# Kernel optimization log

Measured on AMD Instinct MI355X. Metric: run time of the kernel, lower is better.

The kernel has to match this reference:

```python
import jax, jax.numpy as jnp
import numpy as np


def setup_inputs() -> dict:
    key = jax.random.key(0)
    ks = jax.random.split(key, 7)
    B, Nc, Nt = 4, 2048, 2048
    D = 512          # key_size == representation_size
    H, E = 8, 64     # num_heads, head_dim = D // H
    return {
        "keys": jax.random.normal(ks[0], (B, Nc, D), dtype=jnp.float32),
        "values": jax.random.normal(ks[1], (B, Nc, D), dtype=jnp.float32),
        "query": jax.random.normal(ks[2], (B, Nt, D), dtype=jnp.float32),
        "Wk": jax.random.normal(ks[3], (H, D, E), dtype=jnp.float32) * 0.02,
        "Wv": jax.random.normal(ks[4], (H, D, E), dtype=jnp.float32) * 0.02,
        "Wq": jax.random.normal(ks[5], (H, D, E), dtype=jnp.float32) * 0.02,
        "Wout": jax.random.normal(ks[6], (D, D), dtype=jnp.float32) * 0.02,
    }


def reference(keys, values, query, Wk, Wv, Wq, Wout):
    # Batched per-head projections (replaces the per-head Python loop)
    k = jnp.einsum("bnd,hde->bhne", keys, Wk)    # [B,H,Nc,E]
    v = jnp.einsum("bnd,hde->bhne", values, Wv)  # [B,H,Nc,E]
    q = jnp.einsum("bnd,hde->bhne", query, Wq)   # [B,H,Nt,E]
    head_dim = q.shape[-1]
    # NOTE: original scales by head_dim (query.size()[2]), not sqrt(head_dim)
    scores = jnp.einsum("bhqe,bhke->bhqk", q, k) / head_dim
    attn = jax.nn.softmax(scores, axis=-1)
    out = jnp.einsum("bhqk,bhke->bhqe", attn, v)  # [B,H,Nt,E]
    # concat over heads (head-major feature order, matches torch.cat(dim=-1))
    B, H, Nt, E = out.shape
    out = jnp.transpose(out, (0, 2, 1, 3)).reshape(B, Nt, H * E)
    # final Linear (no bias): x @ Wout^T
    return out @ Wout.T
```

## Files before the change

kernel.cpp:

```cpp
#include <hip/hip_runtime.h>

#define B_   4
#define H_   8
#define NSEQ 2048
#define D_   512
#define E_   64

typedef __bf16 bf16x8 __attribute__((ext_vector_type(8)));
typedef float  f32x4  __attribute__((ext_vector_type(4)));
typedef float  f32x16 __attribute__((ext_vector_type(16)));

__device__ __forceinline__ unsigned short f2b(float f) {
    __bf16 h = (__bf16)f;
    return __builtin_bit_cast(unsigned short, h);
}
__device__ __forceinline__ unsigned pk2(float a, float b) {
    return (unsigned)f2b(a) | ((unsigned)f2b(b) << 16);
}
__device__ __forceinline__ bf16x8 ld_frag(const unsigned short* p) {
    return *reinterpret_cast<const bf16x8*>(p);
}
__device__ __forceinline__ void async_copy16(const void* g, const unsigned short* l) {
    __builtin_amdgcn_global_load_lds(
        (const __attribute__((address_space(1))) unsigned int*)g,
        (__attribute__((address_space(3))) unsigned int*)l, 16, 0, 0);
}

__device__ __forceinline__ int lds_blk(int r, int s) {
    int lr = r >> 1;
    return lr * 128 + (((((r & 1) << 3) | s) ^ (lr & 15)) << 3);
}
#define STAGE_SRC(r0, l, row, slot)                                            \
    {   int lr_ = ((r0) >> 1) + ((l) >> 4);                                    \
        int B_x = ((l) & 15) ^ (lr_ & 15);                                     \
        row = (lr_ << 1) | (B_x >> 3);  slot = B_x & 7; }

__global__ __launch_bounds__(256)
void cast_w_kernel(const float* __restrict__ Wk, const float* __restrict__ Wv,
                   const float* __restrict__ Wq, const float* __restrict__ Wo,
                   unsigned short* __restrict__ okt, unsigned short* __restrict__ ovt,
                   unsigned short* __restrict__ oqt, unsigned short* __restrict__ oo) {
    int idx = blockIdx.x * 256 + threadIdx.x;
    int y = blockIdx.y;
    if (y == 3) { oo[idx] = f2b(Wo[idx]); return; }
    const float* src = y == 0 ? Wk : (y == 1 ? Wv : Wq);
    unsigned short* dst = y == 0 ? okt : (y == 1 ? ovt : oqt);
    float scl = (y == 2) ? 0.015625f : 1.0f;
    int hh = idx >> 15, rem = idx & 32767, d = rem >> 6, e = rem & 63;
    dst[hh * 32768 + e * 512 + d] = f2b(src[idx] * scl);
}

__global__ __launch_bounds__(256)
void xcast_kernel(const float* __restrict__ q, const float* __restrict__ k,
                  const float* __restrict__ v,
                  unsigned short* __restrict__ qx, unsigned short* __restrict__ kx,
                  unsigned short* __restrict__ vx) {
    const int y = blockIdx.y;
    const float* src = y == 0 ? q : (y == 1 ? k : v);
    unsigned short* dst = y == 0 ? qx : (y == 1 ? kx : vx);
    #pragma unroll
    for (int i = 0; i < 4; ++i) {
        int e = blockIdx.x * 4096 + i * 1024 + threadIdx.x * 4;
        float4 f = *reinterpret_cast<const float4*>(src + e);
        *reinterpret_cast<ushort4*>(dst + e) =
            make_ushort4(f2b(f.x), f2b(f.y), f2b(f.z), f2b(f.w));
    }
}

__global__ __launch_bounds__(256, 2)
void proj_gemm(const unsigned short* __restrict__ qx,
               const unsigned short* __restrict__ kx,
               const unsigned short* __restrict__ vx,
               const unsigned short* __restrict__ wqt,
               const unsigned short* __restrict__ wkt,
               const unsigned short* __restrict__ wvt,
               unsigned short* __restrict__ qb, unsigned short* __restrict__ kb,
               unsigned short* __restrict__ vtb) {
    const int m0  = blockIdx.x * 128;
    const int no0 = blockIdx.y * 128;
    const int which = blockIdx.z;
    const int tid = threadIdx.x;
    const int wave = tid >> 6, lane = tid & 63;
    const int quad = lane >> 4, l16 = lane & 15;
    const int wr = wave >> 1, wc = wave & 1;

    const unsigned short* X = which == 0 ? qx : (which == 1 ? kx : vx);
    const unsigned short* W = which == 0 ? wqt : (which == 1 ? wkt : wvt);

    __shared__ unsigned short SM[32768];
    unsigned short* Ab = SM;
    unsigned short* Bb = SM + 16384;

    const unsigned short* Xp = X + (size_t)m0 * D_;
    const unsigned short* Wp = W + (size_t)no0 * D_;

    int rowS[4], slS[4];
    #pragma unroll
    for (int i = 0; i < 4; ++i) STAGE_SRC(wave * 32 + i * 8, lane, rowS[i], slS[i])

    #define PROJ_STAGE(kt, buf)                                                \
        {   _Pragma("unroll")                                                  \
            for (int i = 0; i < 4; ++i)                                        \
                async_copy16(Xp + (size_t)rowS[i] * D_ + (kt) * 64 + slS[i] * 8, \
                             Ab + (buf) * 8192 + (wave * 32 + i * 8) * 64);    \
            _Pragma("unroll")                                                  \
            for (int i = 0; i < 4; ++i)                                        \
                async_copy16(Wp + (size_t)rowS[i] * D_ + (kt) * 64 + slS[i] * 8, \
                             Bb + (buf) * 8192 + (wave * 32 + i * 8) * 64);    \
        }

    PROJ_STAGE(0, 0)
    __syncthreads();

    const f32x4 z = {0.f, 0.f, 0.f, 0.f};
    f32x4 acc[4][4];
    #pragma unroll
    for (int i = 0; i < 4; ++i)
        #pragma unroll
        for (int j = 0; j < 4; ++j) acc[i][j] = z;

    for (int kt = 0; kt < 8; ++kt) {
        const int cur = kt & 1;
        if (kt + 1 < 8) PROJ_STAGE(kt + 1, 1 - cur)
        #pragma unroll
        for (int kk = 0; kk < 2; ++kk) {
            const int s = kk * 4 + quad;
            bf16x8 bfr[4];
            #pragma unroll
            for (int nt = 0; nt < 4; ++nt)
                bfr[nt] = ld_frag(&Bb[cur * 8192 +
                                      lds_blk(wc * 64 + nt * 16 + l16, s)]);
            #pragma unroll
            for (int mt = 0; mt < 4; ++mt) {
                bf16x8 af = ld_frag(&Ab[cur * 8192 +
                                        lds_blk(wr * 64 + mt * 16 + l16, s)]);
                #pragma unroll
                for (int nt = 0; nt < 4; ++nt)
                    acc[mt][nt] = __builtin_amdgcn_mfma_f32_16x16x32_bf16(
                        af, bfr[nt], acc[mt][nt], 0, 0, 0);
            }
        }
        __syncthreads();
    }

    if (which != 2) {
        unsigned short (*Os)[136] = reinterpret_cast<unsigned short(*)[136]>(SM);
        #pragma unroll
        for (int mt = 0; mt < 4; ++mt)
            #pragma unroll
            for (int nt = 0; nt < 4; ++nt)
                #pragma unroll
                for (int r = 0; r < 4; ++r)
                    Os[wr * 64 + mt * 16 + quad * 4 + r][wc * 64 + nt * 16 + l16] =
                        f2b(acc[mt][nt][r]);
        __syncthreads();
        unsigned short* Y = (which == 0 ? qb : kb);
        #pragma unroll
        for (int i = 0; i < 8; ++i) {
            int idx = tid + i * 256;
            int row = idx >> 4, seg = idx & 15;
            *reinterpret_cast<uint4*>(Y + (size_t)(m0 + row) * D_ + no0 + seg * 8) =
                *reinterpret_cast<const uint4*>(&Os[row][seg * 8]);
        }
    } else {
        unsigned short (*Ot)[138] = reinterpret_cast<unsigned short(*)[138]>(SM);
        #pragma unroll
        for (int mt = 0; mt < 4; ++mt)
            #pragma unroll
            for (int nt = 0; nt < 4; ++nt) {
                ushort4 o = make_ushort4(f2b(acc[mt][nt][0]), f2b(acc[mt][nt][1]),
                                         f2b(acc[mt][nt][2]), f2b(acc[mt][nt][3]));
                *reinterpret_cast<ushort4*>(
                    &Ot[wc * 64 + nt * 16 + l16][wr * 64 + mt * 16 + quad * 4]) = o;
            }
        __syncthreads();
        const int b = m0 >> 11, nloc = m0 & 2047;
        #pragma unroll
        for (int i = 0; i < 8; ++i) {
            int idx = tid + i * 256;
            int lhe = idx >> 4, seg = idx & 15;
            int ghe = no0 + lhe;
            *reinterpret_cast<uint4*>(
                vtb + ((size_t)(b * H_ + (ghe >> 6)) * E_ + (ghe & 63)) * NSEQ +
                nloc + seg * 8) =
                *reinterpret_cast<const uint4*>(&Ot[lhe][seg * 8]);
        }
    }
    #undef PROJ_STAGE
}

__global__ __launch_bounds__(256, 3)
void attn_kernel(const unsigned short* __restrict__ qbp,
                 const unsigned short* __restrict__ kbp,
                 const unsigned short* __restrict__ vtbp,
                 unsigned short* __restrict__ aob) {
    const int L = blockIdx.x;
    const int bh = L & 31, qt = L >> 5;
    const int b = bh >> 3, h = bh & 7;
    const int n0 = qt * 64;
    const int tid = threadIdx.x;
    const int wave = tid >> 6, lane = tid & 63;
    const int wk = wave >> 1, wq = wave & 1;
    const int l32 = lane & 31, hi = lane >> 5;

    __shared__ unsigned short Ks[2][4096];
    __shared__ unsigned short Vs[2][4096];

    const unsigned short* kbase = kbp + (size_t)(b * NSEQ) * D_ + h * 64;
    const unsigned short* vbase = vtbp + (size_t)(b * H_ + h) * E_ * NSEQ;

    int rowS[2], slS[2];
    #pragma unroll
    for (int i = 0; i < 2; ++i) STAGE_SRC(wave * 16 + i * 8, lane, rowS[i], slS[i])

    bf16x8 qf[4];
    #pragma unroll
    for (int ks = 0; ks < 4; ++ks)
        qf[ks] = ld_frag(qbp + (size_t)(b * NSEQ + n0 + wq * 32 + l32) * D_ +
                         h * 64 + ks * 16 + hi * 8);

    #define ATTN_STAGE(j, buf)                                                 \
        {   _Pragma("unroll")                                                  \
            for (int i = 0; i < 2; ++i) {                                      \
                async_copy16(                                                  \
                    kbase + (size_t)((j) * 64 + rowS[i]) * D_ + slS[i] * 8,    \
                    &Ks[buf][wave * 1024 + i * 512]);                          \
                async_copy16(                                                  \
                    vbase + (size_t)rowS[i] * NSEQ + (j) * 64 + slS[i] * 8,    \
                    &Vs[buf][wave * 1024 + i * 512]);                          \
            } }

    ATTN_STAGE(0, 0)
    __syncthreads();

    f32x16 oacc[2] = {};
    float lacc = 0.f;

    for (int j = 0; j < NSEQ / 64; ++j) {
        const int cur = j & 1;
        if (j + 1 < NSEQ / 64) ATTN_STAGE(j + 1, 1 - cur)

        const unsigned short* Kc = Ks[cur];
        const unsigned short* Vc = Vs[cur];

        f32x16 sacc = {};
        #pragma unroll
        for (int ks = 0; ks < 4; ++ks) {
            bf16x8 kf = ld_frag(&Kc[lds_blk(wk * 32 + l32, ks * 2 + hi)]);
            sacc = __builtin_amdgcn_mfma_f32_32x32x16_bf16(kf, qf[ks], sacc, 0, 0, 0);
        }

        float p[16];
        #pragma unroll
        for (int r = 0; r < 16; ++r) p[r] = __expf(sacc[r]);
        lacc += ((p[0] + p[1]) + (p[2] + p[3])) + ((p[4] + p[5]) + (p[6] + p[7])) +
                (((p[8] + p[9]) + (p[10] + p[11])) + ((p[12] + p[13]) + (p[14] + p[15])));

        #pragma unroll
        for (int s = 0; s < 2; ++s) {
            unsigned x0 = pk2(p[s * 8 + 0], p[s * 8 + 1]);
            unsigned x1 = pk2(p[s * 8 + 2], p[s * 8 + 3]);
            unsigned y0 = pk2(p[s * 8 + 4], p[s * 8 + 5]);
            unsigned y1 = pk2(p[s * 8 + 6], p[s * 8 + 7]);
            asm volatile("v_permlane32_swap_b32 %0, %1" : "+v"(x0), "+v"(y0));
            asm volatile("v_permlane32_swap_b32 %0, %1" : "+v"(x1), "+v"(y1));
            uint4 u = make_uint4(x0, x1, y0, y1);
            bf16x8 pb = __builtin_bit_cast(bf16x8, u);
            #pragma unroll
            for (int eb = 0; eb < 2; ++eb) {
                bf16x8 vf = ld_frag(&Vc[lds_blk(eb * 32 + l32, wk * 4 + s * 2 + hi)]);
                oacc[eb] = __builtin_amdgcn_mfma_f32_32x32x16_bf16(
                    vf, pb, oacc[eb], 0, 0, 0);
            }
        }

        __syncthreads();
    }

    lacc += __shfl_xor(lacc, 32);
    float* Of = reinterpret_cast<float*>(&Ks[0][0]);
    float* Lf = reinterpret_cast<float*>(&Vs[0][0]);
    if (wk == 0) {
        #pragma unroll
        for (int eb = 0; eb < 2; ++eb)
            #pragma unroll
            for (int rg = 0; rg < 4; ++rg) {
                f32x4 v = {oacc[eb][rg * 4 + 0], oacc[eb][rg * 4 + 1],
                           oacc[eb][rg * 4 + 2], oacc[eb][rg * 4 + 3]};
                *reinterpret_cast<f32x4*>(
                    &Of[(wq * 32 + l32) * 64 + eb * 32 + rg * 8 + hi * 4]) = v;
            }
        if (hi == 0) Lf[wq * 32 + l32] = lacc;
    }
    __syncthreads();
    if (wk == 1) {
        const float li = 1.0f / (lacc + Lf[wq * 32 + l32]);
        unsigned short* op =
            aob + (size_t)(b * NSEQ + n0 + wq * 32 + l32) * D_ + h * 64;
        #pragma unroll
        for (int eb = 0; eb < 2; ++eb)
            #pragma unroll
            for (int rg = 0; rg < 4; ++rg) {
                const f32x4 o = *reinterpret_cast<const f32x4*>(
                    &Of[(wq * 32 + l32) * 64 + eb * 32 + rg * 8 + hi * 4]);
                ushort4 st = make_ushort4(f2b((oacc[eb][rg * 4 + 0] + o.x) * li),
                                          f2b((oacc[eb][rg * 4 + 1] + o.y) * li),
                                          f2b((oacc[eb][rg * 4 + 2] + o.z) * li),
                                          f2b((oacc[eb][rg * 4 + 3] + o.w) * li));
                *reinterpret_cast<ushort4*>(op + eb * 32 + rg * 8 + hi * 4) = st;
            }
    }
    #undef ATTN_STAGE
}

__global__ __launch_bounds__(256, 2)
void out_gemm(const unsigned short* __restrict__ A,
              const unsigned short* __restrict__ Wo,
              float* __restrict__ Out) {
    const int m0  = blockIdx.x * 128;
    const int no0 = blockIdx.y * 128;
    const int tid = threadIdx.x;
    const int wave = tid >> 6, lane = tid & 63;
    const int quad = lane >> 4, l16 = lane & 15;
    const int wr = wave >> 1, wc = wave & 1;

    __shared__ unsigned short SM[32768];
    unsigned short* Ab = SM;
    unsigned short* Bb = SM + 16384;

    const unsigned short* Ap = A + (size_t)m0 * D_;
    const unsigned short* Bp = Wo + (size_t)no0 * D_;

    int rowS[4], slS[4];
    #pragma unroll
    for (int i = 0; i < 4; ++i) STAGE_SRC(wave * 32 + i * 8, lane, rowS[i], slS[i])

    #define OUT_STAGE(kt, buf)                                                 \
        {   _Pragma("unroll")                                                  \
            for (int i = 0; i < 4; ++i)                                        \
                async_copy16(Ap + (size_t)rowS[i] * D_ + (kt) * 64 + slS[i] * 8, \
                             Ab + (buf) * 8192 + (wave * 32 + i * 8) * 64);    \
            _Pragma("unroll")                                                  \
            for (int i = 0; i < 4; ++i)                                        \
                async_copy16(Bp + (size_t)rowS[i] * D_ + (kt) * 64 + slS[i] * 8, \
                             Bb + (buf) * 8192 + (wave * 32 + i * 8) * 64);    \
        }

    OUT_STAGE(0, 0)
    __syncthreads();

    const f32x4 z = {0.f, 0.f, 0.f, 0.f};
    f32x4 acc[4][4];
    #pragma unroll
    for (int i = 0; i < 4; ++i)
        #pragma unroll
        for (int j = 0; j < 4; ++j) acc[i][j] = z;

    for (int kt = 0; kt < 8; ++kt) {
        const int cur = kt & 1;
        if (kt + 1 < 8) OUT_STAGE(kt + 1, 1 - cur)
        #pragma unroll
        for (int kk = 0; kk < 2; ++kk) {
            const int s = kk * 4 + quad;
            bf16x8 bfr[4];
            #pragma unroll
            for (int nt = 0; nt < 4; ++nt)
                bfr[nt] = ld_frag(&Bb[cur * 8192 +
                                      lds_blk(wc * 64 + nt * 16 + l16, s)]);
            #pragma unroll
            for (int mt = 0; mt < 4; ++mt) {
                bf16x8 af = ld_frag(&Ab[cur * 8192 +
                                        lds_blk(wr * 64 + mt * 16 + l16, s)]);
                #pragma unroll
                for (int nt = 0; nt < 4; ++nt)
                    acc[mt][nt] = __builtin_amdgcn_mfma_f32_16x16x32_bf16(
                        af, bfr[nt], acc[mt][nt], 0, 0, 0);
            }
        }
        __syncthreads();
    }
    #pragma unroll
    for (int mt = 0; mt < 4; ++mt)
        #pragma unroll
        for (int nt = 0; nt < 4; ++nt)
            #pragma unroll
            for (int r = 0; r < 4; ++r)
                Out[(size_t)(m0 + wr * 64 + mt * 16 + quad * 4 + r) * D_ +
                    no0 + wc * 64 + nt * 16 + l16] = acc[mt][nt][r];
    #undef OUT_STAGE
}

extern "C" void kernel_launch(void* const* d_in, const int* in_sizes, int n_in,
                              void* d_out, int out_size, void* d_ws, size_t ws_size,
                              hipStream_t stream) {
    const float* keys   = (const float*)d_in[0];
    const float* values = (const float*)d_in[1];
    const float* query  = (const float*)d_in[2];
    const float* Wk     = (const float*)d_in[3];
    const float* Wv     = (const float*)d_in[4];
    const float* Wq     = (const float*)d_in[5];
    const float* Wout   = (const float*)d_in[6];
    float* out = (float*)d_out;

    unsigned short* ws16 = (unsigned short*)d_ws;
    const size_t XN = (size_t)B_ * NSEQ * D_;
    const size_t WN = (size_t)H_ * D_ * E_;
    unsigned short* wkt = ws16;
    unsigned short* wvt = wkt + WN;
    unsigned short* wqt = wvt + WN;
    unsigned short* wob = wqt + WN;
    unsigned short* qb  = wob + WN;
    unsigned short* kb  = qb + XN;
    unsigned short* vtb = kb + XN;
    unsigned short* aob = vtb + XN;
    unsigned short* qx  = aob + XN;
    unsigned short* kx  = qx + XN;
    unsigned short* vx  = aob;

    cast_w_kernel<<<dim3(1024, 4), 256, 0, stream>>>(Wk, Wv, Wq, Wout,
                                                     wkt, wvt, wqt, wob);

    xcast_kernel<<<dim3(1024, 3), 256, 0, stream>>>(query, keys, values,
                                                    qx, kx, vx);

    proj_gemm<<<dim3(64, 4, 3), 256, 0, stream>>>(
        qx, kx, vx, wqt, wkt, wvt, qb, kb, vtb);

    attn_kernel<<<dim3(1024), 256, 0, stream>>>(qb, kb, vtb, aob);

    out_gemm<<<dim3(64, 4), 256, 0, stream>>>(aob, wob, out);
}
```

Baseline: 188.0 us.

## Merge cast kernels and halve GEMM K-tile LDS to raise occupancy

Fuses the weight-cast and activation-cast kernels into one launch, with the weight cast folded into a fourth blockIdx.y slice. Both projection and output GEMMs shrink their K-tile from 64 to 32 with a new swizzle, halving shared memory so three blocks can fit per CU, and set launch bounds to match. The epilogues are split into two halves so they fit in the smaller LDS. This trades more loop iterations and barriers for higher occupancy and one fewer kernel launch.

```diff
diff --git a/kernel.cpp b/kernel.cpp
--- a/kernel.cpp
+++ b/kernel.cpp
@@ -35,27 +35,35 @@
         int B_x = ((l) & 15) ^ (lr_ & 15);                                     \
         row = (lr_ << 1) | (B_x >> 3);  slot = B_x & 7; }
 
+__device__ __forceinline__ int lds_blk32(int r, int s) {
+    int lr = r >> 2;
+    return lr * 128 + (((((r & 3) << 2) | s) ^ (lr & 15)) << 3);
+}
+#define STAGE_SRC32(r0, l, row, slot)                                          \
+    {   int lr_ = ((r0) >> 2) + ((l) >> 4);                                    \
+        int B_x = ((l) & 15) ^ (lr_ & 15);                                     \
+        row = (lr_ << 2) | (B_x >> 2);  slot = B_x & 3; }
+
 __global__ __launch_bounds__(256)
-void cast_w_kernel(const float* __restrict__ Wk, const float* __restrict__ Wv,
-                   const float* __restrict__ Wq, const float* __restrict__ Wo,
-                   unsigned short* __restrict__ okt, unsigned short* __restrict__ ovt,
-                   unsigned short* __restrict__ oqt, unsigned short* __restrict__ oo) {
-    int idx = blockIdx.x * 256 + threadIdx.x;
-    int y = blockIdx.y;
-    if (y == 3) { oo[idx] = f2b(Wo[idx]); return; }
-    const float* src = y == 0 ? Wk : (y == 1 ? Wv : Wq);
-    unsigned short* dst = y == 0 ? okt : (y == 1 ? ovt : oqt);
-    float scl = (y == 2) ? 0.015625f : 1.0f;
-    int hh = idx >> 15, rem = idx & 32767, d = rem >> 6, e = rem & 63;
-    dst[hh * 32768 + e * 512 + d] = f2b(src[idx] * scl);
-}
-
-__global__ __launch_bounds__(256)
-void xcast_kernel(const float* __restrict__ q, const float* __restrict__ k,
-                  const float* __restrict__ v,
-                  unsigned short* __restrict__ qx, unsigned short* __restrict__ kx,
-                  unsigned short* __restrict__ vx) {
+void prep_kernel(const float* __restrict__ q, const float* __restrict__ k,
+                 const float* __restrict__ v,
+                 const float* __restrict__ Wk, const float* __restrict__ Wv,
+                 const float* __restrict__ Wq, const float* __restrict__ Wo,
+                 unsigned short* __restrict__ qx, unsigned short* __restrict__ kx,
+                 unsigned short* __restrict__ vx,
+                 unsigned short* __restrict__ okt, unsigned short* __restrict__ ovt,
+                 unsigned short* __restrict__ oqt, unsigned short* __restrict__ oo) {
     const int y = blockIdx.y;
+    if (y == 3) {
+        int idx = blockIdx.x * 256 + threadIdx.x;
+        int hh = idx >> 15, rem = idx & 32767, d = rem >> 6, e = rem & 63;
+        int t = hh * 32768 + e * 512 + d;
+        okt[t] = f2b(Wk[idx]);
+        ovt[t] = f2b(Wv[idx]);
+        oqt[t] = f2b(Wq[idx] * 0.015625f);
+        oo[idx] = f2b(Wo[idx]);
+        return;
+    }
     const float* src = y == 0 ? q : (y == 1 ? k : v);
     unsigned short* dst = y == 0 ? qx : (y == 1 ? kx : vx);
     #pragma unroll
@@ -67,7 +75,7 @@
     }
 }
 
-__global__ __launch_bounds__(256, 2)
+__global__ __launch_bounds__(256, 3)
 void proj_gemm(const unsigned short* __restrict__ qx,
                const unsigned short* __restrict__ kx,
                const unsigned short* __restrict__ vx,
@@ -87,26 +95,26 @@
     const unsigned short* X = which == 0 ? qx : (which == 1 ? kx : vx);
     const unsigned short* W = which == 0 ? wqt : (which == 1 ? wkt : wvt);
 
-    __shared__ unsigned short SM[32768];
+    __shared__ unsigned short SM[16384];
     unsigned short* Ab = SM;
-    unsigned short* Bb = SM + 16384;
+    unsigned short* Bb = SM + 8192;
 
     const unsigned short* Xp = X + (size_t)m0 * D_;
     const unsigned short* Wp = W + (size_t)no0 * D_;
 
-    int rowS[4], slS[4];
-    #pragma unroll
-    for (int i = 0; i < 4; ++i) STAGE_SRC(wave * 32 + i * 8, lane, rowS[i], slS[i])
+    int rowS[2], slS[2];
+    #pragma unroll
+    for (int i = 0; i < 2; ++i) STAGE_SRC32(wave * 32 + i * 16, lane, rowS[i], slS[i])
 
     #define PROJ_STAGE(kt, buf)                                                \
         {   _Pragma("unroll")                                                  \
-            for (int i = 0; i < 4; ++i)                                        \
-                async_copy16(Xp + (size_t)rowS[i] * D_ + (kt) * 64 + slS[i] * 8, \
-                             Ab + (buf) * 8192 + (wave * 32 + i * 8) * 64);    \
+            for (int i = 0; i < 2; ++i)                                        \
+                async_copy16(Xp + (size_t)rowS[i] * D_ + (kt) * 32 + slS[i] * 8, \
+                             Ab + (buf) * 4096 + (wave * 32 + i * 16) * 32);   \
             _Pragma("unroll")                                                  \
-            for (int i = 0; i < 4; ++i)                                        \
-                async_copy16(Wp + (size_t)rowS[i] * D_ + (kt) * 64 + slS[i] * 8, \
-                             Bb + (buf) * 8192 + (wave * 32 + i * 8) * 64);    \
+            for (int i = 0; i < 2; ++i)                                        \
+                async_copy16(Wp + (size_t)rowS[i] * D_ + (kt) * 32 + slS[i] * 8, \
+                             Bb + (buf) * 4096 + (wave * 32 + i * 16) * 32);   \
         }
 
     PROJ_STAGE(0, 0)
@@ -119,71 +127,81 @@
         #pragma unroll
         for (int j = 0; j < 4; ++j) acc[i][j] = z;
 
-    for (int kt = 0; kt < 8; ++kt) {
+    for (int kt = 0; kt < 16; ++kt) {
         const int cur = kt & 1;
-        if (kt + 1 < 8) PROJ_STAGE(kt + 1, 1 - cur)
-        #pragma unroll
-        for (int kk = 0; kk < 2; ++kk) {
-            const int s = kk * 4 + quad;
-            bf16x8 bfr[4];
+        if (kt + 1 < 16) PROJ_STAGE(kt + 1, 1 - cur)
+        bf16x8 bfr[4];
+        #pragma unroll
+        for (int nt = 0; nt < 4; ++nt)
+            bfr[nt] = ld_frag(&Bb[cur * 4096 +
+                                  lds_blk32(wc * 64 + nt * 16 + l16, quad)]);
+        #pragma unroll
+        for (int mt = 0; mt < 4; ++mt) {
+            bf16x8 af = ld_frag(&Ab[cur * 4096 +
+                                    lds_blk32(wr * 64 + mt * 16 + l16, quad)]);
             #pragma unroll
             for (int nt = 0; nt < 4; ++nt)
-                bfr[nt] = ld_frag(&Bb[cur * 8192 +
-                                      lds_blk(wc * 64 + nt * 16 + l16, s)]);
-            #pragma unroll
-            for (int mt = 0; mt < 4; ++mt) {
-                bf16x8 af = ld_frag(&Ab[cur * 8192 +
-                                        lds_blk(wr * 64 + mt * 16 + l16, s)]);
+                acc[mt][nt] = __builtin_amdgcn_mfma_f32_16x16x32_bf16(
+                    af, bfr[nt], acc[mt][nt], 0, 0, 0);
+        }
+        __syncthreads();
+    }
+
+    if (which != 2) {
+        unsigned short* Y = (which == 0 ? qb : kb);
+        unsigned short (*Os)[136] = reinterpret_cast<unsigned short(*)[136]>(SM);
+        #pragma unroll
+        for (int h = 0; h < 2; ++h) {
+            if (wr == h) {
                 #pragma unroll
-                for (int nt = 0; nt < 4; ++nt)
-                    acc[mt][nt] = __builtin_amdgcn_mfma_f32_16x16x32_bf16(
-                        af, bfr[nt], acc[mt][nt], 0, 0, 0);
-            }
-        }
-        __syncthreads();
-    }
-
-    if (which != 2) {
-        unsigned short (*Os)[136] = reinterpret_cast<unsigned short(*)[136]>(SM);
-        #pragma unroll
-        for (int mt = 0; mt < 4; ++mt)
-            #pragma unroll
-            for (int nt = 0; nt < 4; ++nt)
+                for (int mt = 0; mt < 4; ++mt)
+                    #pragma unroll
+                    for (int nt = 0; nt < 4; ++nt)
+                        #pragma unroll
+                        for (int r = 0; r < 4; ++r)
+                            Os[mt * 16 + quad * 4 + r][wc * 64 + nt * 16 + l16] =
+                                f2b(acc[mt][nt][r]);
+            }
+            __syncthreads();
+            #pragma unroll
+            for (int i = 0; i < 4; ++i) {
+                int idx = tid + i * 256;
+                int row = idx >> 4, seg = idx & 15;
+                *reinterpret_cast<uint4*>(
+                    Y + (size_t)(m0 + h * 64 + row) * D_ + no0 + seg * 8) =
+                    *reinterpret_cast<const uint4*>(&Os[row][seg * 8]);
+            }
+            if (h == 0) __syncthreads();
+        }
+    } else {
+        unsigned short (*Ot)[144] = reinterpret_cast<unsigned short(*)[144]>(SM);
+        const int b = m0 >> 11, nloc = m0 & 2047;
+        #pragma unroll
+        for (int h = 0; h < 2; ++h) {
+            if (wc == h) {
                 #pragma unroll
-                for (int r = 0; r < 4; ++r)
-                    Os[wr * 64 + mt * 16 + quad * 4 + r][wc * 64 + nt * 16 + l16] =
-                        f2b(acc[mt][nt][r]);
-        __syncthreads();
-        unsigned short* Y = (which == 0 ? qb : kb);
-        #pragma unroll
-        for (int i = 0; i < 8; ++i) {
-            int idx = tid + i * 256;
-            int row = idx >> 4, seg = idx & 15;
-            *reinterpret_cast<uint4*>(Y + (size_t)(m0 + row) * D_ + no0 + seg * 8) =
-                *reinterpret_cast<const uint4*>(&Os[row][seg * 8]);
-        }
-    } else {
-        unsigned short (*Ot)[138] = reinterpret_cast<unsigned short(*)[138]>(SM);
-        #pragma unroll
-        for (int mt = 0; mt < 4; ++mt)
-            #pragma unroll
-            for (int nt = 0; nt < 4; ++nt) {
-                ushort4 o = make_ushort4(f2b(acc[mt][nt][0]), f2b(acc[mt][nt][1]),
-                                         f2b(acc[mt][nt][2]), f2b(acc[mt][nt][3]));
-                *reinterpret_cast<ushort4*>(
-                    &Ot[wc * 64 + nt * 16 + l16][wr * 64 + mt * 16 + quad * 4]) = o;
-            }
-        __syncthreads();
-        const int b = m0 >> 11, nloc = m0 & 2047;
-        #pragma unroll
-        for (int i = 0; i < 8; ++i) {
-            int idx = tid + i * 256;
-            int lhe = idx >> 4, seg = idx & 15;
-            int ghe = no0 + lhe;
-            *reinterpret_cast<uint4*>(
-                vtb + ((size_t)(b * H_ + (ghe >> 6)) * E_ + (ghe & 63)) * NSEQ +
-                nloc + seg * 8) =
-                *reinterpret_cast<const uint4*>(&Ot[lhe][seg * 8]);
+                for (int mt = 0; mt < 4; ++mt)
+                    #pragma unroll
+                    for (int nt = 0; nt < 4; ++nt) {
+                        ushort4 o = make_ushort4(
+                            f2b(acc[mt][nt][0]), f2b(acc[mt][nt][1]),
+                            f2b(acc[mt][nt][2]), f2b(acc[mt][nt][3]));
+                        *reinterpret_cast<ushort4*>(
+                            &Ot[nt * 16 + l16][wr * 64 + mt * 16 + quad * 4]) = o;
+                    }
+            }
+            __syncthreads();
+            #pragma unroll
+            for (int i = 0; i < 4; ++i) {
+                int idx = tid + i * 256;
+                int lhe = idx >> 4, seg = idx & 15;
+                int ghe = no0 + h * 64 + lhe;
+                *reinterpret_cast<uint4*>(
+                    vtb + ((size_t)(b * H_ + (ghe >> 6)) * E_ + (ghe & 63)) * NSEQ +
+                    nloc + seg * 8) =
+                    *reinterpret_cast<const uint4*>(&Ot[lhe][seg * 8]);
+            }
+            if (h == 0) __syncthreads();
         }
     }
     #undef PROJ_STAGE
@@ -313,7 +331,7 @@
     #undef ATTN_STAGE
 }
 
-__global__ __launch_bounds__(256, 2)
+__global__ __launch_bounds__(256, 3)
 void out_gemm(const unsigned short* __restrict__ A,
               const unsigned short* __restrict__ Wo,
               float* __restrict__ Out) {
@@ -324,26 +342,26 @@
     const int quad = lane >> 4, l16 = lane & 15;
     const int wr = wave >> 1, wc = wave & 1;
 
-    __shared__ unsigned short SM[32768];
+    __shared__ unsigned short SM[16384];
     unsigned short* Ab = SM;
-    unsigned short* Bb = SM + 16384;
+    unsigned short* Bb = SM + 8192;
 
     const unsigned short* Ap = A + (size_t)m0 * D_;
     const unsigned short* Bp = Wo + (size_t)no0 * D_;
 
-    int rowS[4], slS[4];
-    #pragma unroll
-    for (int i = 0; i < 4; ++i) STAGE_SRC(wave * 32 + i * 8, lane, rowS[i], slS[i])
+    int rowS[2], slS[2];
+    #pragma unroll
+    for (int i = 0; i < 2; ++i) STAGE_SRC32(wave * 32 + i * 16, lane, rowS[i], slS[i])
 
     #define OUT_STAGE(kt, buf)                                                 \
         {   _Pragma("unroll")                                                  \
-            for (int i = 0; i < 4; ++i)                                        \
-                async_copy16(Ap + (size_t)rowS[i] * D_ + (kt) * 64 + slS[i] * 8, \
-                             Ab + (buf) * 8192 + (wave * 32 + i * 8) * 64);    \
+            for (int i = 0; i < 2; ++i)                                        \
+                async_copy16(Ap + (size_t)rowS[i] * D_ + (kt) * 32 + slS[i] * 8, \
+                             Ab + (buf) * 4096 + (wave * 32 + i * 16) * 32);   \
             _Pragma("unroll")                                                  \
-            for (int i = 0; i < 4; ++i)                                        \
-                async_copy16(Bp + (size_t)rowS[i] * D_ + (kt) * 64 + slS[i] * 8, \
-                             Bb + (buf) * 8192 + (wave * 32 + i * 8) * 64);    \
+            for (int i = 0; i < 2; ++i)                                        \
+                async_copy16(Bp + (size_t)rowS[i] * D_ + (kt) * 32 + slS[i] * 8, \
+                             Bb + (buf) * 4096 + (wave * 32 + i * 16) * 32);   \
         }
 
     OUT_STAGE(0, 0)
@@ -356,26 +374,22 @@
         #pragma unroll
         for (int j = 0; j < 4; ++j) acc[i][j] = z;
 
-    for (int kt = 0; kt < 8; ++kt) {
+    for (int kt = 0; kt < 16; ++kt) {
         const int cur = kt & 1;
-        if (kt + 1 < 8) OUT_STAGE(kt + 1, 1 - cur)
-        #pragma unroll
-        for (int kk = 0; kk < 2; ++kk) {
-            const int s = kk * 4 + quad;
-            bf16x8 bfr[4];
+        if (kt + 1 < 16) OUT_STAGE(kt + 1, 1 - cur)
+        bf16x8 bfr[4];
+        #pragma unroll
+        for (int nt = 0; nt < 4; ++nt)
+            bfr[nt] = ld_frag(&Bb[cur * 4096 +
+                                  lds_blk32(wc * 64 + nt * 16 + l16, quad)]);
+        #pragma unroll
+        for (int mt = 0; mt < 4; ++mt) {
+            bf16x8 af = ld_frag(&Ab[cur * 4096 +
+                                    lds_blk32(wr * 64 + mt * 16 + l16, quad)]);
             #pragma unroll
             for (int nt = 0; nt < 4; ++nt)
-                bfr[nt] = ld_frag(&Bb[cur * 8192 +
-                                      lds_blk(wc * 64 + nt * 16 + l16, s)]);
-            #pragma unroll
-            for (int mt = 0; mt < 4; ++mt) {
-                bf16x8 af = ld_frag(&Ab[cur * 8192 +
-                                        lds_blk(wr * 64 + mt * 16 + l16, s)]);
-                #pragma unroll
-                for (int nt = 0; nt < 4; ++nt)
-                    acc[mt][nt] = __builtin_amdgcn_mfma_f32_16x16x32_bf16(
-                        af, bfr[nt], acc[mt][nt], 0, 0, 0);
-            }
+                acc[mt][nt] = __builtin_amdgcn_mfma_f32_16x16x32_bf16(
+                    af, bfr[nt], acc[mt][nt], 0, 0, 0);
         }
         __syncthreads();
     }
@@ -417,11 +431,9 @@
     unsigned short* kx  = qx + XN;
     unsigned short* vx  = aob;
 
-    cast_w_kernel<<<dim3(1024, 4), 256, 0, stream>>>(Wk, Wv, Wq, Wout,
-                                                     wkt, wvt, wqt, wob);
-
-    xcast_kernel<<<dim3(1024, 3), 256, 0, stream>>>(query, keys, values,
-                                                    qx, kx, vx);
+    prep_kernel<<<dim3(1024, 4), 256, 0, stream>>>(
+        query, keys, values, Wk, Wv, Wq, Wout,
+        qx, kx, vx, wkt, wvt, wqt, wob);
 
     proj_gemm<<<dim3(64, 4, 3), 256, 0, stream>>>(
         qx, kx, vx, wqt, wkt, wvt, qb, kb, vtb);
```

Measured after the change: 187.4 us. Within noise of the previous version (-0.4%).
